# Kernel tuning notes

Hardware: AMD Instinct MI355X
Metric: run time of the kernel (lower is better)

## Reference

```python
import jax, jax.numpy as jnp
import numpy as np

D_MODEL = 1024
H = 16
D_K = D_MODEL // H
D_FF = 4096
EPS = 1e-6
NEG = -1e9


def layer_norm(x, alpha, beta):
    # Custom LN: scalar alpha/beta, unbiased std, eps added to std (not var)
    mean = jnp.mean(x, axis=-1, keepdims=True)
    std = jnp.std(x, axis=-1, ddof=1, keepdims=True)
    return alpha * (x - mean) / (std + EPS) + beta


def setup_inputs() -> dict:
    key = jax.random.key(0)
    ks = jax.random.split(key, 16)
    B, S = 4, 2048
    s = 1.0 / np.sqrt(D_MODEL)
    inp = {
        "x": jax.random.normal(ks[0], (B, S, D_MODEL), dtype=jnp.float32),
        "src_mask": jax.random.randint(ks[1], (B, 1, 1, S), 0, 2, dtype=jnp.int32),
        "wq": jax.random.normal(ks[2], (D_MODEL, D_MODEL), jnp.float32) * s,
        "bq": jnp.zeros((D_MODEL,), jnp.float32),
        "wk": jax.random.normal(ks[3], (D_MODEL, D_MODEL), jnp.float32) * s,
        "bk": jnp.zeros((D_MODEL,), jnp.float32),
        "wv": jax.random.normal(ks[4], (D_MODEL, D_MODEL), jnp.float32) * s,
        "bv": jnp.zeros((D_MODEL,), jnp.float32),
        "wo": jax.random.normal(ks[5], (D_MODEL, D_MODEL), jnp.float32) * s,
        "bo": jnp.zeros((D_MODEL,), jnp.float32),
        "w1": jax.random.normal(ks[6], (D_MODEL, D_FF), jnp.float32) * s,
        "b1": jnp.zeros((D_FF,), jnp.float32),
        "w2": jax.random.normal(ks[7], (D_FF, D_MODEL), jnp.float32) * (1.0 / np.sqrt(D_FF)),
        "b2": jnp.zeros((D_MODEL,), jnp.float32),
        "a1": jnp.ones((1,), jnp.float32),
        "be1": jnp.zeros((1,), jnp.float32),
        "a2": jnp.ones((1,), jnp.float32),
        "be2": jnp.zeros((1,), jnp.float32),
    }
    return inp


def reference(x, src_mask, wq, bq, wk, bk, wv, bv, wo, bo, w1, b1, w2, b2, a1, be1, a2, be2):
    B, S, _ = x.shape

    # --- residual 1: self-attention on pre-LN input (dropout = identity, eval) ---
    xn = layer_norm(x, a1, be1)
    q = (xn @ wq + bq).reshape(B, S, H, D_K).transpose(0, 2, 1, 3)  # [B,H,S,Dk]
    k = (xn @ wk + bk).reshape(B, S, H, D_K).transpose(0, 2, 1, 3)
    v = (xn @ wv + bv).reshape(B, S, H, D_K).transpose(0, 2, 1, 3)

    scores = jnp.einsum("bhqd,bhkd->bhqk", q, k) / jnp.sqrt(jnp.float32(D_K))
    scores = jnp.where(src_mask == 0, jnp.float32(NEG), scores)
    attn = jax.nn.softmax(scores, axis=-1)
    ctx = jnp.einsum("bhqk,bhkd->bhqd", attn, v)  # [B,H,S,Dk]
    ctx = ctx.transpose(0, 2, 1, 3).reshape(B, S, D_MODEL)
    attn_out = ctx @ wo + bo
    x = x + attn_out

    # --- residual 2: feed-forward on pre-LN input ---
    xn2 = layer_norm(x, a2, be2)
    ff = jax.nn.relu(xn2 @ w1 + b1) @ w2 + b2
    return x + ff
```

## Files before the change

kernel.cpp:

```cpp
#include <hip/hip_runtime.h>
#include <stdint.h>

typedef unsigned short u16;
typedef __attribute__((ext_vector_type(8))) short short8;
typedef __attribute__((ext_vector_type(4))) float f32x4;
typedef __attribute__((ext_vector_type(4))) u16 u16x4;
typedef __attribute__((ext_vector_type(4))) uint32_t u32x4;

#define NB 4
#define SEQ 2048
#define DM 1024
#define NH 16
#define DKh 64
#define DFF 4096
#define LOG2E 1.44269504089f

__device__ __forceinline__ u16 f2bf(float f) {
  union { float f; uint32_t u; } v; v.f = f;
  uint32_t u = v.u;
  return (u16)((u + 0x7FFFu + ((u >> 16) & 1u)) >> 16);
}

__device__ __forceinline__ uint32_t cvtpk(float lo, float hi) {
  uint32_t r;
  asm("v_cvt_pk_bf16_f32 %0, %1, %2" : "=v"(r) : "v"(lo), "v"(hi));
  return r;
}

__device__ __forceinline__ float fexp2(float x) {
  float r;
  asm("v_exp_f32 %0, %1" : "=v"(r) : "v"(x));
  return r;
}

__device__ __forceinline__ void gl16(const u16* g, u16* l) {
  __builtin_amdgcn_global_load_lds((const __attribute__((address_space(1))) void*)g,
                                   (__attribute__((address_space(3))) void*)l, 16, 0, 0);
}

__global__ __launch_bounds__(256) void prep(const float* __restrict__ wq, const float* __restrict__ wk,
                                            const float* __restrict__ wv, const float* __restrict__ wo,
                                            const float* __restrict__ w1, const float* __restrict__ w2,
                                            u16* __restrict__ wqT, u16* __restrict__ wkT,
                                            u16* __restrict__ wvT, u16* __restrict__ woT,
                                            u16* __restrict__ w1T, u16* __restrict__ w2T,
                                            const float* __restrict__ bq, const float* __restrict__ bk,
                                            const float* __restrict__ bv, float* __restrict__ bcat) {
  int idx = blockIdx.x;
  int tx = threadIdx.x, ty = threadIdx.y;
  if (idx >= 12288) {
    int i = (idx - 12288) * 256 + ty * 32 + tx;
    if (i < 3072) bcat[i] = (i < 1024) ? bq[i] : ((i < 2048) ? bk[i - 1024] : bv[i - 2048]);
    return;
  }
  const float* src; u16* dst; int R, C, bx, by;
  if (idx < 4096) {
    int z = idx >> 10;
    src = (z == 0) ? wq : (z == 1) ? wk : (z == 2) ? wv : wo;
    dst = (z == 0) ? wqT : (z == 1) ? wkT : (z == 2) ? wvT : woT;
    R = DM; C = DM; int i = idx & 1023; bx = i & 31; by = i >> 5;
  } else if (idx < 8192) {
    src = w1; dst = w1T; R = DM; C = DFF; int i = idx - 4096; bx = i & 127; by = i >> 7;
  } else {
    src = w2; dst = w2T; R = DFF; C = DM; int i = idx - 8192; bx = i & 31; by = i >> 5;
  }
  __shared__ float tile[32][33];
  int c0 = bx * 32, r0 = by * 32;
#pragma unroll
  for (int i = 0; i < 32; i += 8)
    tile[ty + i][tx] = src[(size_t)(r0 + ty + i) * C + c0 + tx];
  __syncthreads();
#pragma unroll
  for (int i = 0; i < 32; i += 8)
    dst[(size_t)(c0 + ty + i) * R + r0 + tx] = f2bf(tile[tx][ty + i]);
}

__global__ __launch_bounds__(1024) void compact_idx(const int* __restrict__ msk,
                                                    int* __restrict__ pinv,
                                                    int* __restrict__ lArr,
                                                    int* __restrict__ lpArr,
                                                    float* __restrict__ fbbc) {
  int b = blockIdx.x;
  int t = threadIdx.x;
  int lane = t & 63, w = t >> 6;
  int i0 = t * 2, i1 = t * 2 + 1;
  int m0 = msk[b * SEQ + i0] ? 1 : 0;
  int m1 = msk[b * SEQ + i1] ? 1 : 0;
  int s = m0 + m1;
  int run = s;
#pragma unroll
  for (int d = 1; d < 64; d <<= 1) {
    int v = __shfl_up(run, d);
    if (lane >= d) run += v;
  }
  __shared__ int wtot[16];
  __shared__ int woff[17];
  if (lane == 63) wtot[w] = run;
  __syncthreads();
  if (t == 0) {
    int acc = 0;
#pragma unroll
    for (int i = 0; i < 16; ++i) { woff[i] = acc; acc += wtot[i]; }
    woff[16] = acc;
  }
  __syncthreads();
  int excl = run - s + woff[w];
  pinv[b * SEQ + i0] = m0 ? excl : -1;
  pinv[b * SEQ + i1] = m1 ? (excl + m0) : -1;
  int L = woff[16];
  if (t == 0) {
    lArr[b] = L;
    int LP = (L + 63) & ~63;
    if (LP == 0) LP = 64;
    lpArr[b] = LP;
  }
  for (int l = t; l < SEQ; l += 1024)
    fbbc[b * SEQ + l] = (l < L) ? 0.0f : -1e9f;
}

__global__ __launch_bounds__(256) void ln_bf16(const float* __restrict__ x,
                                               u16* __restrict__ out,
                                               const float* __restrict__ alpha,
                                               const float* __restrict__ beta) {
  int row = blockIdx.x;
  const float4* xr = (const float4*)(x + (size_t)row * DM);
  int t = threadIdx.x;
  float4 v = xr[t];
  float s = v.x + v.y + v.z + v.w;
  float s2 = v.x * v.x + v.y * v.y + v.z * v.z + v.w * v.w;
#pragma unroll
  for (int m = 1; m < 64; m <<= 1) { s += __shfl_xor(s, m); s2 += __shfl_xor(s2, m); }
  __shared__ float red[8];
  int wid = t >> 6, lane = t & 63;
  if (lane == 0) { red[wid] = s; red[wid + 4] = s2; }
  __syncthreads();
  float S = red[0] + red[1] + red[2] + red[3];
  float S2 = red[4] + red[5] + red[6] + red[7];
  float mean = S * (1.0f / DM);
  float var = fmaxf((S2 - S * mean) * (1.0f / (DM - 1)), 0.0f);
  float inv = alpha[0] / (sqrtf(var) + 1e-6f);
  float bet = beta[0];
  u16x4 o;
  o[0] = f2bf((v.x - mean) * inv + bet);
  o[1] = f2bf((v.y - mean) * inv + bet);
  o[2] = f2bf((v.z - mean) * inv + bet);
  o[3] = f2bf((v.w - mean) * inv + bet);
  *(u16x4*)(out + (size_t)row * DM + t * 4) = o;
}

template <int MODE>
__global__ __launch_bounds__(512, 4) void gemm_v2(const u16* __restrict__ A,
                                                  const u16* __restrict__ WT,
                                                  const float* __restrict__ bias,
                                                  const float* __restrict__ resid,
                                                  void* __restrict__ outp,
                                                  const int* __restrict__ pinv,
                                                  int M, int N, int K, float qscale) {
  extern __shared__ u16 lds[];
  int tid = threadIdx.x;
  int lane = tid & 63, wid = tid >> 6;
  int lr = lane & 15, lg = lane >> 4;
  int wr = wid >> 1, wc = wid & 1;
  int nbx = N >> 7;
  int nwg = (M >> 8) * nbx;
  int lid = blockIdx.x;
  int swz = (lid & 7) * (nwg >> 3) + (lid >> 3);
  int m0 = (swz / nbx) << 8, n0 = (swz % nbx) << 7;

  int sr = tid >> 2;
  int sch = tid & 3;
  int scs = sch ^ ((sr >> 1) & 3);
  size_t a_src = (size_t)(m0 + sr) * K + scs * 8;
  size_t b_src = (size_t)(n0 + sr) * K + scs * 8;
  u16* a_dst = lds + sr * 32 + sch * 8;
  u16* b_dst = lds + 8192 + sr * 32 + sch * 8;

#define STAGE(B_, T_) do { \
    gl16(A + a_src + (size_t)(T_) * 32, a_dst + (B_) * 12288); \
    gl16(A + a_src + (size_t)128 * K + (size_t)(T_) * 32, a_dst + (B_) * 12288 + 4096); \
    gl16(WT + b_src + (size_t)(T_) * 32, b_dst + (B_) * 12288); \
  } while (0)

  int rchunk = (lg ^ ((lr >> 1) & 3)) * 8;
  int offA[4], offB[4];
#pragma unroll
  for (int i = 0; i < 4; ++i) offA[i] = (wr * 64 + i * 16 + lr) * 32 + rchunk;
#pragma unroll
  for (int j = 0; j < 4; ++j) offB[j] = 8192 + (wc * 64 + j * 16 + lr) * 32 + rchunk;

  f32x4 acc[4][4] = {};

  int NT = K >> 5;
  STAGE(0, 0);
  STAGE(1, 1);
  asm volatile("s_waitcnt vmcnt(3)" ::: "memory");
  __builtin_amdgcn_s_barrier();

  int buf = 0;
  for (int t = 0; t < NT; ++t) {
    const u16* la = lds + buf * 12288;
    int b2 = buf - 1; if (b2 < 0) b2 += 3;
    short8 af[4], bfr[4];
#pragma unroll
    for (int i = 0; i < 4; ++i) af[i] = *(const short8*)&la[offA[i]];
#pragma unroll
    for (int j = 0; j < 4; ++j) bfr[j] = *(const short8*)&la[offB[j]];
    if (t + 2 < NT) STAGE(b2, t + 2);
    __builtin_amdgcn_s_setprio(1);
#pragma unroll
    for (int i = 0; i < 4; ++i)
#pragma unroll
      for (int j = 0; j < 4; ++j)
        acc[i][j] = __builtin_amdgcn_mfma_f32_16x16x32_bf16(af[i], bfr[j], acc[i][j], 0, 0, 0);
    __builtin_amdgcn_s_setprio(0);
    if (t < NT - 2) asm volatile("s_waitcnt vmcnt(3)" ::: "memory");
    else            asm volatile("s_waitcnt vmcnt(0)" ::: "memory");
    __builtin_amdgcn_s_barrier();
    __builtin_amdgcn_sched_barrier(0);
    buf = (buf == 2) ? 0 : buf + 1;
  }
#undef STAGE

#pragma unroll
  for (int i = 0; i < 4; ++i) {
#pragma unroll
    for (int j = 0; j < 4; ++j) {
      int col = n0 + wc * 64 + j * 16 + lr;
      float bi = bias[col];
      int rbase = m0 + wr * 64 + i * 16 + lg * 4;
      if (MODE == 2) {
        float* o = (float*)outp;
#pragma unroll
        for (int r = 0; r < 4; ++r) {
          size_t idx = (size_t)(rbase + r) * N + col;
          o[idx] = resid[idx] + acc[i][j][r] + bi;
        }
      } else if (MODE == 3) {
        u16* o = (u16*)outp;
#pragma unroll
        for (int r = 0; r < 4; ++r)
          o[(size_t)(rbase + r) * N + col] = f2bf(fmaxf(acc[i][j][r] + bi, 0.0f));
      } else {
        u16* qb = (u16*)outp;
        int which = col >> 10, nc = col & 1023;
        int hh = nc >> 6, dd = nc & 63;
        int bb = rbase >> 11, ss = rbase & 2047;
        if (which == 0) {
#pragma unroll
          for (int r = 0; r < 4; ++r)
            qb[((size_t)(bb * NH + hh) * SEQ + (ss + r)) * DKh + dd] = f2bf((acc[i][j][r] + bi) * qscale);
        } else {
          int4 p4 = *(const int4*)(pinv + bb * SEQ + ss);
          int pos[4] = {p4.x, p4.y, p4.z, p4.w};
          if (which == 1) {
            u16* kcb = qb + (size_t)(8u << 20);
#pragma unroll
            for (int r = 0; r < 4; ++r)
              if (pos[r] >= 0)
                kcb[((size_t)(bb * NH + hh) * SEQ + pos[r]) * DKh + dd] = f2bf(acc[i][j][r] + bi);
          } else {
            u16* vcb = qb + (size_t)2 * (8u << 20);
#pragma unroll
            for (int r = 0; r < 4; ++r)
              if (pos[r] >= 0) {
                int l = pos[r];
                int lo = l & 63;
                int pi = ((lo >> 4) & 1) * 32 + ((lo >> 2) & 3) * 8 + (lo >> 5) * 4 + (lo & 3);
                vcb[((size_t)(bb * NH + hh) * DKh + dd) * SEQ + (l & ~63) + pi] = f2bf(acc[i][j][r] + bi);
              }
          }
        }
      }
    }
  }
}

__global__ __launch_bounds__(512) void attn_fwd(const u16* __restrict__ q,
                                                const u16* __restrict__ kc,
                                                const u16* __restrict__ vc,
                                                const int* __restrict__ lArr,
                                                const int* __restrict__ lpArr,
                                                const float* __restrict__ fbbc,
                                                u16* __restrict__ ctx) {
  __shared__ u16 lds[2][16384];
  int tid = threadIdx.x;
  int wid = tid >> 6, lane = tid & 63;
  int lr = lane & 15, lg = lane >> 4;
  int bh = blockIdx.x;
  int b = bh >> 4, hh = bh & 15;
  int q0 = blockIdx.y * 256 + wid * 32;
  const u16* qbase = q + (size_t)bh * SEQ * DKh;
  const u16* kcb = kc + (size_t)bh * SEQ * DKh;
  const u16* vcb = vc + (size_t)bh * DKh * SEQ;
  const float* fbbase = fbbc + b * SEQ;
  int Lb = lArr[b];
  int LP = lpArr[b];

  short8 qf[2][2];
#pragma unroll
  for (int i = 0; i < 2; ++i)
#pragma unroll
    for (int kk = 0; kk < 2; ++kk)
      qf[i][kk] = *(const short8*)(qbase + (size_t)(q0 + i * 16 + lr) * DKh + kk * 32 + lg * 8);

  int srow = tid >> 3;
  int schk = tid & 7;
  int ks0 = srow * 64 + ((schk ^ (srow & 7)) * 8);
  int vs0 = srow * SEQ + ((schk ^ (srow & 7)) * 8);
  int dst0 = tid * 8;

#define STAGE(B_, KV0) do { \
    gl16(kcb + (size_t)(KV0) * 64 + ks0, &lds[B_][dst0]); \
    gl16(kcb + (size_t)((KV0) + 64) * 64 + ks0, &lds[B_][dst0 + 4096]); \
    gl16(vcb + (size_t)(KV0) + vs0, &lds[B_][dst0 + 8192]); \
    gl16(vcb + (size_t)(KV0) + 64 + vs0, &lds[B_][dst0 + 12288]); \
  } while (0)

  int swzc = (lr & 7) << 3;

  f32x4 ot[2][4] = {};
  float mrow[2] = {-3e38f, -3e38f};
  float lsum[2] = {0.0f, 0.0f};

  STAGE(0, 0);
  asm volatile("s_waitcnt vmcnt(0)" ::: "memory");
  __builtin_amdgcn_s_barrier();

  int buf = 0;
  for (int kv0 = 0; kv0 < LP; kv0 += 128) {
    bool more = (kv0 + 128 < LP);
    if (more) STAGE(buf ^ 1, kv0 + 128);
    if (more) asm volatile("s_waitcnt vmcnt(4)" ::: "memory");
    else      asm volatile("s_waitcnt vmcnt(0)" ::: "memory");
    __builtin_amdgcn_s_barrier();

#pragma unroll
    for (int sB = 0; sB < 2; ++sB) {
      const u16* Ks = &lds[buf][sB * 4096];
      const u16* Vs = &lds[buf][8192 + sB * 4096];
      int kvs = kv0 + sB * 64;

      f32x4 st[2][4] = {};
      __builtin_amdgcn_s_setprio(1);
#pragma unroll
      for (int kk = 0; kk < 2; ++kk) {
        short8 kf[4];
#pragma unroll
        for (int j = 0; j < 4; ++j)
          kf[j] = *(const short8*)&Ks[(j * 16 + lr) * 64 + ((kk * 32 + lg * 8) ^ swzc)];
#pragma unroll
        for (int i = 0; i < 2; ++i)
#pragma unroll
          for (int j = 0; j < 4; ++j)
            st[i][j] = __builtin_amdgcn_mfma_f32_16x16x32_bf16(kf[j], qf[i][kk], st[i][j], 0, 0, 0);
      }
      __builtin_amdgcn_s_setprio(0);

      bool tail = (kvs + 64 > Lb);

      u32x4 pa[2][2];
#pragma unroll
      for (int i = 0; i < 2; ++i) {
        float p[4][4];
        if (tail) {
#pragma unroll
          for (int j = 0; j < 4; ++j) {
            float4 f4 = *(const float4*)(fbbase + kvs + j * 16 + lg * 4);
            p[j][0] = st[i][j][0] + f4.x;
            p[j][1] = st[i][j][1] + f4.y;
            p[j][2] = st[i][j][2] + f4.z;
            p[j][3] = st[i][j][3] + f4.w;
          }
        } else {
#pragma unroll
          for (int j = 0; j < 4; ++j)
#pragma unroll
            for (int r = 0; r < 4; ++r) p[j][r] = st[i][j][r];
        }
        float mx = -3e38f;
#pragma unroll
        for (int j = 0; j < 4; ++j)
#pragma unroll
          for (int r = 0; r < 4; ++r) mx = fmaxf(mx, p[j][r]);
        mx = fmaxf(mx, __shfl_xor(mx, 16));
        mx = fmaxf(mx, __shfl_xor(mx, 32));
        float mnew = fmaxf(mrow[i], mx);
        if (!__all(mnew - mrow[i] <= 8.0f)) {
          float corr = fexp2(mrow[i] - mnew);
          lsum[i] *= corr;
#pragma unroll
          for (int jd = 0; jd < 4; ++jd)
#pragma unroll
            for (int r = 0; r < 4; ++r) ot[i][jd][r] *= corr;
          mrow[i] = mnew;
        }
        float ps = 0.0f;
#pragma unroll
        for (int j = 0; j < 4; ++j)
#pragma unroll
          for (int r = 0; r < 4; ++r) {
            float pv = fexp2(p[j][r] - mrow[i]);
            p[j][r] = pv;
            ps += pv;
          }
        ps += __shfl_xor(ps, 16);
        ps += __shfl_xor(ps, 32);
        lsum[i] += ps;
#pragma unroll
        for (int ks = 0; ks < 2; ++ks) {
          pa[i][ks][0] = cvtpk(p[ks][0], p[ks][1]);
          pa[i][ks][1] = cvtpk(p[ks][2], p[ks][3]);
          pa[i][ks][2] = cvtpk(p[ks + 2][0], p[ks + 2][1]);
          pa[i][ks][3] = cvtpk(p[ks + 2][2], p[ks + 2][3]);
        }
      }

      __builtin_amdgcn_s_setprio(1);
#pragma unroll
      for (int ks = 0; ks < 2; ++ks) {
        short8 vf[4];
#pragma unroll
        for (int jd = 0; jd < 4; ++jd)
          vf[jd] = *(const short8*)&Vs[(jd * 16 + lr) * 64 + ((ks * 32 + lg * 8) ^ swzc)];
#pragma unroll
        for (int i = 0; i < 2; ++i)
#pragma unroll
          for (int jd = 0; jd < 4; ++jd)
            ot[i][jd] = __builtin_amdgcn_mfma_f32_16x16x32_bf16(vf[jd], *(short8*)&pa[i][ks], ot[i][jd], 0, 0, 0);
      }
      __builtin_amdgcn_s_setprio(0);
    }
    __builtin_amdgcn_s_barrier();
    buf ^= 1;
  }
#undef STAGE

  asm volatile("s_waitcnt vmcnt(0)" ::: "memory");
  __builtin_amdgcn_s_barrier();

  float inv0 = 1.0f / lsum[0], inv1 = 1.0f / lsum[1];
  u16* ep = &lds[0][wid * 2048];
#pragma unroll
  for (int i = 0; i < 2; ++i) {
    float inv = i ? inv1 : inv0;
#pragma unroll
    for (int jd = 0; jd < 4; ++jd) {
      uint32_t w0 = cvtpk(ot[i][jd][0] * inv, ot[i][jd][1] * inv);
      uint32_t w1 = cvtpk(ot[i][jd][2] * inv, ot[i][jd][3] * inv);
      uint32_t pk2[2] = {w0, w1};
      *(u16x4*)&ep[(i * 16 + lr) * 64 + ((jd * 16 + lg * 4) ^ swzc)] = *(u16x4*)pk2;
    }
  }
  __syncthreads();
  int q_ = lane >> 1;
  size_t orow = ((size_t)b * SEQ + q0 + q_) * DM + hh * DKh;
#pragma unroll
  for (int it = 0; it < 4; ++it) {
    int dc = (lane & 1) * 32 + it * 8;
    short8 vv = *(const short8*)&ep[q_ * 64 + (dc ^ ((q_ & 7) << 3))];
    *(short8*)(ctx + orow + dc) = vv;
  }
}

extern "C" void kernel_launch(void* const* d_in, const int* in_sizes, int n_in,
                              void* d_out, int out_size, void* d_ws, size_t ws_size,
                              hipStream_t stream) {
  const float* x   = (const float*)d_in[0];
  const int*   msk = (const int*)d_in[1];
  const float* wq  = (const float*)d_in[2];
  const float* bq  = (const float*)d_in[3];
  const float* wk  = (const float*)d_in[4];
  const float* bk  = (const float*)d_in[5];
  const float* wv  = (const float*)d_in[6];
  const float* bv  = (const float*)d_in[7];
  const float* wo  = (const float*)d_in[8];
  const float* bo  = (const float*)d_in[9];
  const float* w1  = (const float*)d_in[10];
  const float* b1  = (const float*)d_in[11];
  const float* w2  = (const float*)d_in[12];
  const float* b2  = (const float*)d_in[13];
  const float* a1  = (const float*)d_in[14];
  const float* be1 = (const float*)d_in[15];
  const float* a2  = (const float*)d_in[16];
  const float* be2 = (const float*)d_in[17];
  float* out = (float*)d_out;

  u16* wqT = (u16*)d_ws;
  u16* wkT = wqT + (1u << 20);
  u16* wvT = wkT + (1u << 20);
  u16* woT = wvT + (1u << 20);
  u16* w1T = woT + (1u << 20);
  u16* w2T = w1T + (4u << 20);
  u16* xn  = w2T + (4u << 20);
  u16* qb  = xn  + (8u << 20);
  u16* kb  = qb  + (8u << 20);
  u16* vtb = kb  + (8u << 20);
  u16* ctx = vtb + (8u << 20);
  u16* hb  = qb;
  float* bcat = (float*)ctx;
  int*   pinv = (int*)(ctx + (8u << 20));
  int*   lArr = pinv + NB * SEQ;
  int*   lpArr = lArr + 16;
  float* fbbc = (float*)(lpArr + 16);

  (void)hipFuncSetAttribute((const void*)gemm_v2<0>, hipFuncAttributeMaxDynamicSharedMemorySize, 72 * 1024);
  (void)hipFuncSetAttribute((const void*)gemm_v2<2>, hipFuncAttributeMaxDynamicSharedMemorySize, 72 * 1024);
  (void)hipFuncSetAttribute((const void*)gemm_v2<3>, hipFuncAttributeMaxDynamicSharedMemorySize, 72 * 1024);

  dim3 tb(32, 8);
  prep<<<12300, tb, 0, stream>>>(wq, wk, wv, wo, w1, w2, wqT, wkT, wvT, woT, w1T, w2T, bq, bk, bv, bcat);
  compact_idx<<<NB, 1024, 0, stream>>>(msk, pinv, lArr, lpArr, fbbc);

  ln_bf16<<<NB * SEQ, 256, 0, stream>>>(x, xn, a1, be1);

  gemm_v2<0><<<768, 512, 72 * 1024, stream>>>(xn, wqT, bcat, nullptr, qb, pinv, NB * SEQ, 3 * DM, DM, 0.125f * LOG2E);

  attn_fwd<<<dim3(NB * NH, SEQ / 256), 512, 0, stream>>>(qb, kb, vtb, lArr, lpArr, fbbc, ctx);

  gemm_v2<2><<<256, 512, 72 * 1024, stream>>>(ctx, woT, bo, x, out, nullptr, NB * SEQ, DM, DM, 1.0f);

  ln_bf16<<<NB * SEQ, 256, 0, stream>>>(out, xn, a2, be2);

  gemm_v2<3><<<1024, 512, 72 * 1024, stream>>>(xn, w1T, b1, nullptr, hb, nullptr, NB * SEQ, DFF, DM, 1.0f);

  gemm_v2<2><<<256, 512, 72 * 1024, stream>>>(hb, w2T, b2, out, out, nullptr, NB * SEQ, DM, DFF, 1.0f);
}
```

Before: 343.7 us.

## Add 256x256-tile 8-wave ping-pong GEMM for QKV and FFN1 projections

Adds a new GEMM kernel with 256x256 output tiles, 8 waves arranged 2x4, and 128KB of double-buffered LDS. It interleaves quarter-tile MFMA blocks with staggered global-to-LDS loads and barriers, using priority raising around the MFMAs. The QKV and FFN1 GEMMs now use it, halving grid size and raising arithmetic intensity per loaded byte. The cost is occupancy of one block per CU, a large accumulator register footprint, and many barriers. The old gemm_v2 keeps only the residual mode.

```diff
diff --git a/kernel.cpp b/kernel.cpp
--- a/kernel.cpp
+++ b/kernel.cpp
@@ -146,6 +146,178 @@
   o[2] = f2bf((v.z - mean) * inv + bet);
   o[3] = f2bf((v.w - mean) * inv + bet);
   *(u16x4*)(out + (size_t)row * DM + t * 4) = o;
+}
+
+template <int MODE>
+__global__ __launch_bounds__(512, 1) void gemm8p(const u16* __restrict__ A,
+                                                 const u16* __restrict__ WT,
+                                                 const float* __restrict__ bias,
+                                                 u16* __restrict__ outp,
+                                                 const int* __restrict__ pinv,
+                                                 int M, int N, int K, float qscale) {
+  extern __shared__ u16 lds[];
+  int tid = threadIdx.x;
+  int lane = tid & 63, wid = tid >> 6;
+  int lr = lane & 15, lg = lane >> 4;
+  int wr = wid >> 2, wc = wid & 3;
+  int nbx = N >> 8;
+  int nwg = (M >> 8) * nbx;
+  int lid = blockIdx.x;
+  int swz = (lid & 7) * (nwg >> 3) + (lid >> 3);
+  int m0 = (swz / nbx) << 8, n0 = (swz % nbx) << 8;
+
+  int srow = tid >> 3, schk = tid & 7;
+  int csrc8 = (schk ^ (srow & 7)) * 8;
+  size_t aS = (size_t)(m0 + srow) * K + csrc8;
+  size_t bS = (size_t)(n0 + srow) * K + csrc8;
+  int dst8 = tid * 8;
+
+#define SGA(D_, H_, T_) do { \
+    const u16* s_ = A + aS + (size_t)(H_) * 128 * K + (size_t)(T_) * 64; \
+    gl16(s_,                  lds + (D_) * 32768 + (H_) * 8192 + dst8); \
+    gl16(s_ + (size_t)64 * K, lds + (D_) * 32768 + (H_) * 8192 + dst8 + 4096); \
+  } while (0)
+#define SGB(D_, H_, T_) do { \
+    const u16* s_ = WT + bS + (size_t)(H_) * 128 * K + (size_t)(T_) * 64; \
+    gl16(s_,                  lds + (D_) * 32768 + 16384 + (H_) * 8192 + dst8); \
+    gl16(s_ + (size_t)64 * K, lds + (D_) * 32768 + 16384 + (H_) * 8192 + dst8 + 4096); \
+  } while (0)
+
+  int ck0 = (lg ^ (lr & 7)) * 8;
+  int ck1 = ((4 + lg) ^ (lr & 7)) * 8;
+  int arow[4], brow[2];
+#pragma unroll
+  for (int i = 0; i < 4; ++i) arow[i] = (i * 32 + wr * 16 + lr) << 6;
+#pragma unroll
+  for (int j = 0; j < 2; ++j) brow[j] = (j * 64 + wc * 16 + lr) << 6;
+
+#define RDA(D_, IH_) do { const u16* p_ = lds + (D_) * 32768 + (IH_) * 8192; \
+    _Pragma("unroll") for (int i_ = 0; i_ < 4; ++i_) { \
+      a_[i_][0] = *(const short8*)&p_[arow[i_] + ck0]; \
+      a_[i_][1] = *(const short8*)&p_[arow[i_] + ck1]; } } while (0)
+#define RDB(D_, JH_, B_) do { const u16* p_ = lds + (D_) * 32768 + 16384 + (JH_) * 8192; \
+    _Pragma("unroll") for (int j_ = 0; j_ < 2; ++j_) { \
+      B_[j_][0] = *(const short8*)&p_[brow[j_] + ck0]; \
+      B_[j_][1] = *(const short8*)&p_[brow[j_] + ck1]; } } while (0)
+#define MMQ(I0_, J0_, B_) do { \
+    _Pragma("unroll") for (int i_ = 0; i_ < 4; ++i_) \
+    _Pragma("unroll") for (int j_ = 0; j_ < 2; ++j_) { \
+      acc[(I0_) + i_][(J0_) + j_] = __builtin_amdgcn_mfma_f32_16x16x32_bf16(a_[i_][0], B_[j_][0], acc[(I0_) + i_][(J0_) + j_], 0, 0, 0); \
+      acc[(I0_) + i_][(J0_) + j_] = __builtin_amdgcn_mfma_f32_16x16x32_bf16(a_[i_][1], B_[j_][1], acc[(I0_) + i_][(J0_) + j_], 0, 0, 0); \
+    } } while (0)
+#define BAR() __builtin_amdgcn_s_barrier()
+#define SBR() __builtin_amdgcn_sched_barrier(0)
+#define PRIO1() __builtin_amdgcn_s_setprio(1)
+#define PRIO0() __builtin_amdgcn_s_setprio(0)
+
+  f32x4 acc[8][4] = {};
+  short8 a_[4][2], b0_[2][2], b1_[2][2];
+
+  int NT = K >> 6;
+  SGA(0, 0, 0); SGB(0, 0, 0); SGB(0, 1, 0); SGA(0, 1, 0);
+  SGA(1, 0, 1); SGB(1, 0, 1); SGB(1, 1, 1);
+  asm volatile("s_waitcnt vmcnt(6)" ::: "memory");
+  BAR();
+
+  int HALF = NT >> 1;
+  for (int I = 0; I < HALF; ++I) {
+    bool s2 = (2 * I + 2 < NT);
+    RDA(0, 0); RDB(0, 0, b0_);
+    SGA(1, 1, 2 * I + 1);
+    BAR();
+    PRIO1(); MMQ(0, 0, b0_); PRIO0();
+    BAR(); SBR();
+    RDB(0, 1, b1_);
+    if (s2) SGA(0, 0, 2 * I + 2);
+    BAR();
+    PRIO1(); MMQ(0, 2, b1_); PRIO0();
+    BAR(); SBR();
+    RDA(0, 1);
+    if (s2) SGB(0, 0, 2 * I + 2);
+    BAR();
+    PRIO1(); MMQ(4, 2, b1_); PRIO0();
+    BAR(); SBR();
+    if (s2) SGB(0, 1, 2 * I + 2);
+    BAR();
+    PRIO1(); MMQ(4, 0, b0_); PRIO0();
+    if (s2) asm volatile("s_waitcnt vmcnt(6)" ::: "memory");
+    else    asm volatile("s_waitcnt vmcnt(0)" ::: "memory");
+    BAR(); SBR();
+    RDA(1, 0); RDB(1, 0, b0_);
+    if (s2) SGA(0, 1, 2 * I + 2);
+    BAR();
+    PRIO1(); MMQ(0, 0, b0_); PRIO0();
+    BAR(); SBR();
+    RDB(1, 1, b1_);
+    if (s2) SGA(1, 0, 2 * I + 3);
+    BAR();
+    PRIO1(); MMQ(0, 2, b1_); PRIO0();
+    BAR(); SBR();
+    RDA(1, 1);
+    if (s2) SGB(1, 0, 2 * I + 3);
+    BAR();
+    PRIO1(); MMQ(4, 2, b1_); PRIO0();
+    BAR(); SBR();
+    if (s2) SGB(1, 1, 2 * I + 3);
+    BAR();
+    PRIO1(); MMQ(4, 0, b0_); PRIO0();
+    if (s2) asm volatile("s_waitcnt vmcnt(6)" ::: "memory");
+    else    asm volatile("s_waitcnt vmcnt(0)" ::: "memory");
+    BAR(); SBR();
+  }
+#undef SGA
+#undef SGB
+#undef RDA
+#undef RDB
+#undef MMQ
+#undef BAR
+#undef SBR
+#undef PRIO1
+#undef PRIO0
+
+#pragma unroll
+  for (int I8 = 0; I8 < 8; ++I8) {
+#pragma unroll
+    for (int J4 = 0; J4 < 4; ++J4) {
+      int col = n0 + (J4 >> 1) * 128 + (J4 & 1) * 64 + wc * 16 + lr;
+      float bi = bias[col];
+      int rbase = m0 + (I8 >> 2) * 128 + (I8 & 3) * 32 + wr * 16 + lg * 4;
+      if (MODE == 3) {
+#pragma unroll
+        for (int r = 0; r < 4; ++r)
+          outp[(size_t)(rbase + r) * N + col] = f2bf(fmaxf(acc[I8][J4][r] + bi, 0.0f));
+      } else {
+        int which = col >> 10, nc = col & 1023;
+        int hh = nc >> 6, dd = nc & 63;
+        int bb = rbase >> 11, ss = rbase & 2047;
+        if (which == 0) {
+#pragma unroll
+          for (int r = 0; r < 4; ++r)
+            outp[((size_t)(bb * NH + hh) * SEQ + (ss + r)) * DKh + dd] = f2bf((acc[I8][J4][r] + bi) * qscale);
+        } else {
+          int4 p4 = *(const int4*)(pinv + bb * SEQ + ss);
+          int pos[4] = {p4.x, p4.y, p4.z, p4.w};
+          if (which == 1) {
+            u16* kcb = outp + (size_t)(8u << 20);
+#pragma unroll
+            for (int r = 0; r < 4; ++r)
+              if (pos[r] >= 0)
+                kcb[((size_t)(bb * NH + hh) * SEQ + pos[r]) * DKh + dd] = f2bf(acc[I8][J4][r] + bi);
+          } else {
+            u16* vcb = outp + (size_t)2 * (8u << 20);
+#pragma unroll
+            for (int r = 0; r < 4; ++r)
+              if (pos[r] >= 0) {
+                int l = pos[r];
+                int lo = l & 63;
+                int pi = ((lo >> 4) & 1) * 32 + ((lo >> 2) & 3) * 8 + (lo >> 5) * 4 + (lo & 3);
+                vcb[((size_t)(bb * NH + hh) * DKh + dd) * SEQ + (l & ~63) + pi] = f2bf(acc[I8][J4][r] + bi);
+              }
+          }
+        }
+      }
+    }
+  }
 }
 
 template <int MODE>
@@ -228,48 +400,11 @@
       int col = n0 + wc * 64 + j * 16 + lr;
       float bi = bias[col];
       int rbase = m0 + wr * 64 + i * 16 + lg * 4;
-      if (MODE == 2) {
-        float* o = (float*)outp;
-#pragma unroll
-        for (int r = 0; r < 4; ++r) {
-          size_t idx = (size_t)(rbase + r) * N + col;
-          o[idx] = resid[idx] + acc[i][j][r] + bi;
-        }
-      } else if (MODE == 3) {
-        u16* o = (u16*)outp;
-#pragma unroll
-        for (int r = 0; r < 4; ++r)
-          o[(size_t)(rbase + r) * N + col] = f2bf(fmaxf(acc[i][j][r] + bi, 0.0f));
-      } else {
-        u16* qb = (u16*)outp;
-        int which = col >> 10, nc = col & 1023;
-        int hh = nc >> 6, dd = nc & 63;
-        int bb = rbase >> 11, ss = rbase & 2047;
-        if (which == 0) {
-#pragma unroll
-          for (int r = 0; r < 4; ++r)
-            qb[((size_t)(bb * NH + hh) * SEQ + (ss + r)) * DKh + dd] = f2bf((acc[i][j][r] + bi) * qscale);
-        } else {
-          int4 p4 = *(const int4*)(pinv + bb * SEQ + ss);
-          int pos[4] = {p4.x, p4.y, p4.z, p4.w};
-          if (which == 1) {
-            u16* kcb = qb + (size_t)(8u << 20);
-#pragma unroll
-            for (int r = 0; r < 4; ++r)
-              if (pos[r] >= 0)
-                kcb[((size_t)(bb * NH + hh) * SEQ + pos[r]) * DKh + dd] = f2bf(acc[i][j][r] + bi);
-          } else {
-            u16* vcb = qb + (size_t)2 * (8u << 20);
-#pragma unroll
-            for (int r = 0; r < 4; ++r)
-              if (pos[r] >= 0) {
-                int l = pos[r];
-                int lo = l & 63;
-                int pi = ((lo >> 4) & 1) * 32 + ((lo >> 2) & 3) * 8 + (lo >> 5) * 4 + (lo & 3);
-                vcb[((size_t)(bb * NH + hh) * DKh + dd) * SEQ + (l & ~63) + pi] = f2bf(acc[i][j][r] + bi);
-              }
-          }
-        }
+      float* o = (float*)outp;
+#pragma unroll
+      for (int r = 0; r < 4; ++r) {
+        size_t idx = (size_t)(rbase + r) * N + col;
+        o[idx] = resid[idx] + acc[i][j][r] + bi;
       }
     }
   }
@@ -503,9 +638,9 @@
   int*   lpArr = lArr + 16;
   float* fbbc = (float*)(lpArr + 16);
 
-  (void)hipFuncSetAttribute((const void*)gemm_v2<0>, hipFuncAttributeMaxDynamicSharedMemorySize, 72 * 1024);
+  (void)hipFuncSetAttribute((const void*)gemm8p<0>, hipFuncAttributeMaxDynamicSharedMemorySize, 128 * 1024);
+  (void)hipFuncSetAttribute((const void*)gemm8p<3>, hipFuncAttributeMaxDynamicSharedMemorySize, 128 * 1024);
   (void)hipFuncSetAttribute((const void*)gemm_v2<2>, hipFuncAttributeMaxDynamicSharedMemorySize, 72 * 1024);
-  (void)hipFuncSetAttribute((const void*)gemm_v2<3>, hipFuncAttributeMaxDynamicSharedMemorySize, 72 * 1024);
 
   dim3 tb(32, 8);
   prep<<<12300, tb, 0, stream>>>(wq, wk, wv, wo, w1, w2, wqT, wkT, wvT, woT, w1T, w2T, bq, bk, bv, bcat);
@@ -513,7 +648,7 @@
 
   ln_bf16<<<NB * SEQ, 256, 0, stream>>>(x, xn, a1, be1);
 
-  gemm_v2<0><<<768, 512, 72 * 1024, stream>>>(xn, wqT, bcat, nullptr, qb, pinv, NB * SEQ, 3 * DM, DM, 0.125f * LOG2E);
+  gemm8p<0><<<384, 512, 128 * 1024, stream>>>(xn, wqT, bcat, qb, pinv, NB * SEQ, 3 * DM, DM, 0.125f * LOG2E);
 
   attn_fwd<<<dim3(NB * NH, SEQ / 256), 512, 0, stream>>>(qb, kb, vtb, lArr, lpArr, fbbc, ctx);
 
@@ -521,7 +656,7 @@
 
   ln_bf16<<<NB * SEQ, 256, 0, stream>>>(out, xn, a2, be2);
 
-  gemm_v2<3><<<1024, 512, 72 * 1024, stream>>>(xn, w1T, b1, nullptr, hb, nullptr, NB * SEQ, DFF, DM, 1.0f);
+  gemm8p<3><<<512, 512, 128 * 1024, stream>>>(xn, w1T, b1, hb, nullptr, NB * SEQ, DFF, DM, 1.0f);
 
   gemm_v2<2><<<256, 512, 72 * 1024, stream>>>(hb, w2T, b2, out, out, nullptr, NB * SEQ, DM, DFF, 1.0f);
 }
```

After: 354.6 us. +3.2%, slower.
